# Performance work log

Measured on AMD Instinct MI355X. Metric: run time of the kernel, lower is better.

The kernel has to match this reference:

```python
import jax, jax.numpy as jnp
import numpy as np

N = 30000
E = 960000
F_IN = 16
NH1 = 36
NH2 = 36
KH = 8
IN_POOL = 2
OUT_POOL = 2
NUM_CLASSES = 10
RATIO = 0.1
EPS = 1e-5


def cheb_conv(x, src, dst, valid, W, b):
    """PyG ChebConv with sym normalization, lambda_max=2 -> L_hat = -D^-1/2 A D^-1/2.
    W: [K, in, out], valid: float mask [E] for (soft-)deleted edges."""
    n = x.shape[0]
    deg = jax.ops.segment_sum(valid, src, num_segments=n)
    dinv = jnp.where(deg > 0, jax.lax.rsqrt(deg), 0.0)
    norm = dinv[src] * dinv[dst] * valid  # [E]

    def prop(h):  # L_hat @ h
        return -jax.ops.segment_sum(norm[:, None] * h[src], dst, num_segments=n)

    k_hops = W.shape[0]
    tx0 = x
    out = tx0 @ W[0]
    if k_hops > 1:
        tx1 = prop(tx0)
        out = out + tx1 @ W[1]
        for kk in range(2, k_hops):
            tx2 = 2.0 * prop(tx1) - tx0
            out = out + tx2 @ W[kk]
            tx0, tx1 = tx1, tx2
    return out + b


def batch_norm(x, gamma, beta):
    mu = jnp.mean(x, axis=0)
    var = jnp.var(x, axis=0)
    return (x - mu) * jax.lax.rsqrt(var + EPS) * gamma + beta


def setup_inputs() -> dict:
    key = jax.random.key(0)
    ks = jax.random.split(key, 20)
    rn = lambda k, s: jax.random.normal(k, s, dtype=jnp.float32) * 0.1
    x = jax.random.normal(ks[0], (N, F_IN), dtype=jnp.float32)
    edge_index = jax.random.randint(ks[1], (2, E), 0, N, dtype=jnp.int32)
    return {
        "x": x,
        "edge_index": edge_index,
        "W1": rn(ks[2], (KH, F_IN, NH1)), "b1": jnp.zeros((NH1,), jnp.float32),
        "W2": rn(ks[3], (KH, NH1, NH2)), "b2": jnp.zeros((NH2,), jnp.float32),
        "g1": jnp.ones((NH1,), jnp.float32), "be1": jnp.zeros((NH1,), jnp.float32),
        "g2": jnp.ones((NH2,), jnp.float32), "be2": jnp.zeros((NH2,), jnp.float32),
        "Wc": rn(ks[4], (1, NH1, IN_POOL)), "bc": jnp.zeros((IN_POOL,), jnp.float32),
        "pool_w": rn(ks[5], (IN_POOL,)),
        "Wp": rn(ks[6], (KH, IN_POOL, OUT_POOL)), "bp": jnp.zeros((OUT_POOL,), jnp.float32),
        "W3": rn(ks[7], (1, NH1 + NH2 + OUT_POOL, NUM_CLASSES)),
        "b3": jnp.zeros((NUM_CLASSES,), jnp.float32),
    }


def reference(x, edge_index, W1, b1, W2, b2, g1, be1, g2, be2, Wc, bc, pool_w, Wp, bp, W3, b3):
    src, dst = edge_index[0], edge_index[1]
    valid = jnp.ones((src.shape[0],), jnp.float32)

    x1 = batch_norm(jax.nn.relu(cheb_conv(x, src, dst, valid, W1, b1)), g1, be1)
    x2 = batch_norm(jax.nn.relu(cheb_conv(x1, src, dst, valid, W2, b2)), g2, be2)
    xc = cheb_conv(x1, src, dst, valid, Wc, bc)

    # TopKPooling(ratio=0.1)
    score = jnp.tanh(xc @ pool_w / jnp.linalg.norm(pool_w))  # [N]
    k = int(np.ceil(RATIO * x.shape[0]))
    _, perm = jax.lax.top_k(score, k)
    xp1 = xc[perm] * score[perm][:, None]
    new_idx = jnp.full((x.shape[0],), -1, jnp.int32).at[perm].set(jnp.arange(k, dtype=jnp.int32))
    vs, vd = new_idx[src], new_idx[dst]
    valid_p = ((vs >= 0) & (vd >= 0)).astype(jnp.float32)
    src_p = jnp.where(vs >= 0, vs, 0)
    dst_p = jnp.where(vd >= 0, vd, 0)

    xp2 = cheb_conv(xp1, src_p, dst_p, valid_p, Wp, bp)  # [k, OUT_POOL]

    # nearest-neighbor unpooling using last-2 feature columns as 2D positions
    pos = x[:, -2:]              # [N, 2]
    pos_p = pos[perm]            # [k, 2]
    d2 = jnp.sum((pos[:, None, :] - pos_p[None, :, :]) ** 2, axis=-1)  # [N, k]
    nearest = jnp.argmin(d2, axis=1)
    x3u = xp2[nearest]           # [N, OUT_POOL]

    h = jnp.concatenate((x1, x2, x3u), axis=1)
    return cheb_conv(h, src, dst, valid, W3, b3)
```

## Files before the change

kernel.cpp:

```cpp
#include <hip/hip_runtime.h>
#include <cstdint>

constexpr int NN   = 30000;
constexpr int NE   = 960000;
constexpr int FIN  = 16;
constexpr int H1   = 36;
constexpr int H2   = 36;
constexpr int KHOP = 8;
constexpr int KSEL = 3000;
constexpr int PCAP = 32768;
constexpr int NCHUNK = 12;
constexpr int CHUNK = KSEL / NCHUNK;
constexpr int NB_H = 32;
constexpr int EPB  = (NE + NB_H - 1) / NB_H;
constexpr float EPSV = 1e-5f;

#define TPB 256

static inline int nb(long long t) { return (int)((t + TPB - 1) / TPB); }

__global__ __launch_bounds__(1024)
void k_hist(const int* __restrict__ src, const int* __restrict__ dst,
            int* __restrict__ partials, int* __restrict__ rank) {
    __shared__ int hist[NN];
    for (int j = threadIdx.x; j < NN; j += 1024) hist[j] = 0;
    __syncthreads();
    int b = blockIdx.x;
    int e0 = b * EPB, e1 = min(NE, e0 + EPB);
    if (blockIdx.y == 0) {
        for (int e = e0 + (int)threadIdx.x; e < e1; e += 1024)
            atomicAdd(&hist[src[e]], 1);
    } else {
        for (int e = e0 + (int)threadIdx.x; e < e1; e += 1024)
            rank[e] = atomicAdd(&hist[dst[e]], 1);
    }
    __syncthreads();
    int* P = partials + ((size_t)blockIdx.y * NB_H + b) * NN;
    for (int j = threadIdx.x; j < NN; j += 1024) P[j] = hist[j];
}

__global__ void k_red(int* __restrict__ partials, float* __restrict__ dinv,
                      int* __restrict__ cnt_dst, float* __restrict__ stats) {
    if (blockIdx.x == 0 && threadIdx.x < 144) stats[threadIdx.x] = 0.f;
    int j = blockIdx.x * blockDim.x + threadIdx.x;
    if (j >= NN) return;
    const int* Ps = partials;
    int s = 0;
#pragma unroll
    for (int b = 0; b < NB_H; ++b) s += Ps[(size_t)b * NN + j];
    dinv[j] = s > 0 ? rsqrtf((float)s) : 0.0f;
    int* Pd = partials + (size_t)NB_H * NN;
    int run = 0;
#pragma unroll
    for (int b = 0; b < NB_H; ++b) {
        int t = Pd[(size_t)b * NN + j];
        Pd[(size_t)b * NN + j] = run;
        run += t;
    }
    cnt_dst[j] = run;
}

__device__ __forceinline__ int block_scan_excl_1024(int val, int& total) {
    __shared__ int wsum[16];
    int tid = threadIdx.x, lane = tid & 63, wv = tid >> 6;
    int v = val;
#pragma unroll
    for (int off = 1; off < 64; off <<= 1) {
        int t = __shfl_up(v, off, 64);
        if (lane >= off) v += t;
    }
    __syncthreads();
    if (lane == 63) wsum[wv] = v;
    __syncthreads();
    if (tid < 16) {
        int w = wsum[tid];
#pragma unroll
        for (int off = 1; off < 16; off <<= 1) {
            int t = __shfl_up(w, off, 64);
            if (tid >= off) w += t;
        }
        wsum[tid] = w;
    }
    __syncthreads();
    int base = (wv > 0) ? wsum[wv - 1] : 0;
    total = wsum[15];
    return base + v - val;
}

__global__ void k_scan(const int* __restrict__ cnt, int* __restrict__ rowstart, int n) {
    __shared__ int run;
    if (threadIdx.x == 0) run = 0;
    __syncthreads();
    for (int base = 0; base < n; base += 1024) {
        int i = base + threadIdx.x;
        int v = (i < n) ? cnt[i] : 0;
        int tot; int ex = block_scan_excl_1024(v, tot);
        int r = run;
        if (i < n) rowstart[i] = r + ex;
        __syncthreads();
        if (threadIdx.x == 0) run += tot;
        __syncthreads();
    }
    if (threadIdx.x == 0) rowstart[n] = run;
}

__global__ __launch_bounds__(1024)
void k_scan_pool(const int* __restrict__ lens, int* __restrict__ prs,
                 const int* __restrict__ pcnt, float* __restrict__ dinvp) {
    __shared__ int run;
    if (threadIdx.x == 0) run = 0;
    __syncthreads();
    for (int base = 0; base < KSEL; base += 1024) {
        int i = base + threadIdx.x;
        int v = (i < KSEL) ? lens[i] : 0;
        int tot; int ex = block_scan_excl_1024(v, tot);
        int r = run;
        if (i < KSEL) prs[i] = r + ex;
        __syncthreads();
        if (threadIdx.x == 0) run += tot;
        __syncthreads();
    }
    if (threadIdx.x == 0) prs[KSEL] = run;
    for (int j = threadIdx.x; j < KSEL; j += 1024) {
        int c = pcnt[j];
        dinvp[j] = c > 0 ? rsqrtf((float)c) : 0.0f;
    }
}

__global__ void k_fill3(const int* __restrict__ src, const int* __restrict__ dst,
                        const int* __restrict__ rank, const float* __restrict__ dinv,
                        const int* __restrict__ rowstart, const int* __restrict__ Pd_excl,
                        int2* __restrict__ csr, int E) {
    int e = blockIdx.x * blockDim.x + threadIdx.x;
    if (e >= E) return;
    int s = src[e], d = dst[e];
    int b = e / EPB;
    int pos = rowstart[d] + Pd_excl[(size_t)b * NN + d] + rank[e];
    float w = -dinv[s] * dinv[d];
    csr[pos] = make_int2(s, __float_as_int(w));
}

template<int F, int O, int BN, int ES, bool FIRST>
__global__ __launch_bounds__(BN * (F / 4) * ES)
void k_prop_gemm(const int* __restrict__ rowstart, const int2* __restrict__ csr,
                 const float* __restrict__ h, const float* __restrict__ t0,
                 const float* __restrict__ Wk, const float* __restrict__ W0,
                 const float* __restrict__ bias, float* __restrict__ tout,
                 float* __restrict__ acc, int n) {
    constexpr int QF = F / 4;
    constexpr int NTH = BN * QF;
    constexpr int NT = NTH * ES;
    __shared__ float sT[BN * F];
    __shared__ float sP[(ES > 1) ? BN * F : 1];
    __shared__ float sW[F * O];
    __shared__ float sW0[FIRST ? F * O : 1];
    __shared__ float sX[FIRST ? BN * F : 1];
    const int tid = threadIdx.x;
    for (int i = tid; i < F * O; i += NT) sW[i] = Wk[i];
    if (FIRST) {
        for (int i = tid; i < F * O; i += NT) sW0[i] = W0[i];
        int base = blockIdx.x * BN * F;
        int lim = min(BN * F, n * F - base);
        for (int i = tid; i < lim; i += NT) sX[i] = h[base + i];
    }
    const int sl = tid / NTH;
    const int t2 = tid - sl * NTH;
    const int nl = t2 / QF, q = t2 - nl * QF;
    const int node = blockIdx.x * BN + nl;
    float4 p = {0.f, 0.f, 0.f, 0.f};
    if (node < n) {
        const float4* __restrict__ h4 = (const float4*)h;
        int e0 = rowstart[node], e1 = rowstart[node + 1];
        if (ES > 1) {
            int len = e1 - e0, half = (len + 1) >> 1;
            if (sl == 0) e1 = e0 + half; else e0 += half;
        }
        int e = e0;
        for (; e + 3 < e1; e += 4) {
            int2 ea = csr[e];
            int2 eb = csr[e + 1];
            int2 ec = csr[e + 2];
            int2 ed = csr[e + 3];
            float4 ha = h4[ea.x * QF + q];
            float4 hb = h4[eb.x * QF + q];
            float4 hc = h4[ec.x * QF + q];
            float4 hd = h4[ed.x * QF + q];
            float wa = __int_as_float(ea.y), wb = __int_as_float(eb.y);
            float wc = __int_as_float(ec.y), wd = __int_as_float(ed.y);
            p.x = fmaf(wa, ha.x, p.x); p.y = fmaf(wa, ha.y, p.y);
            p.z = fmaf(wa, ha.z, p.z); p.w = fmaf(wa, ha.w, p.w);
            p.x = fmaf(wb, hb.x, p.x); p.y = fmaf(wb, hb.y, p.y);
            p.z = fmaf(wb, hb.z, p.z); p.w = fmaf(wb, hb.w, p.w);
            p.x = fmaf(wc, hc.x, p.x); p.y = fmaf(wc, hc.y, p.y);
            p.z = fmaf(wc, hc.z, p.z); p.w = fmaf(wc, hc.w, p.w);
            p.x = fmaf(wd, hd.x, p.x); p.y = fmaf(wd, hd.y, p.y);
            p.z = fmaf(wd, hd.z, p.z); p.w = fmaf(wd, hd.w, p.w);
        }
        for (; e < e1; ++e) {
            int2 ew = csr[e];
            float w = __int_as_float(ew.y);
            float4 hv = h4[ew.x * QF + q];
            p.x = fmaf(w, hv.x, p.x); p.y = fmaf(w, hv.y, p.y);
            p.z = fmaf(w, hv.z, p.z); p.w = fmaf(w, hv.w, p.w);
        }
    }
    if (ES > 1) {
        if (sl == 1 && node < n) {
            sP[nl * F + 4 * q + 0] = p.x; sP[nl * F + 4 * q + 1] = p.y;
            sP[nl * F + 4 * q + 2] = p.z; sP[nl * F + 4 * q + 3] = p.w;
        }
        __syncthreads();
        if (sl == 0 && node < n) {
            p.x += sP[nl * F + 4 * q + 0]; p.y += sP[nl * F + 4 * q + 1];
            p.z += sP[nl * F + 4 * q + 2]; p.w += sP[nl * F + 4 * q + 3];
        }
    }
    if (sl == 0 && node < n) {
        if (!FIRST) {
            float4 tv = ((const float4*)t0)[node * QF + q];
            p.x = 2.f * p.x - tv.x; p.y = 2.f * p.y - tv.y;
            p.z = 2.f * p.z - tv.z; p.w = 2.f * p.w - tv.w;
        }
        ((float4*)tout)[node * QF + q] = p;
        sT[nl * F + 4 * q + 0] = p.x; sT[nl * F + 4 * q + 1] = p.y;
        sT[nl * F + 4 * q + 2] = p.z; sT[nl * F + 4 * q + 3] = p.w;
    }
    __syncthreads();
    for (int idx = tid; idx < BN * O; idx += NT) {
        int nl2 = idx / O, o = idx - nl2 * O;
        int gn = blockIdx.x * BN + nl2;
        if (gn >= n) break;
        float s;
        if (FIRST) {
            s = bias[o];
#pragma unroll
            for (int f = 0; f < F; ++f) s = fmaf(sX[nl2 * F + f], sW0[f * O + o], s);
        } else {
            s = 0.f;
        }
#pragma unroll
        for (int f = 0; f < F; ++f) s = fmaf(sT[nl2 * F + f], sW[f * O + o], s);
        if (FIRST) acc[gn * O + o] = s;
        else       acc[gn * O + o] += s;
    }
}

template<int C>
__global__ void k_colstats(const float* __restrict__ a, float* __restrict__ stats, int n) {
    __shared__ float b1[C], b2[C];
    for (int i = threadIdx.x; i < C; i += blockDim.x) { b1[i] = 0.f; b2[i] = 0.f; }
    __syncthreads();
    int t0 = blockIdx.x * blockDim.x + threadIdx.x;
    int stride = gridDim.x * blockDim.x;
    int c = t0 % C;
    float s1 = 0.f, s2 = 0.f;
    for (int t = t0; t < n * C; t += stride) {
        float v = fmaxf(a[t], 0.f);
        s1 += v; s2 = fmaf(v, v, s2);
    }
    atomicAdd(&b1[c], s1); atomicAdd(&b2[c], s2);
    __syncthreads();
    for (int i = threadIdx.x; i < C; i += blockDim.x) {
        atomicAdd(&stats[i], b1[i]); atomicAdd(&stats[C + i], b2[i]);
    }
}

template<int C>
__global__ void k_bn(const float* __restrict__ a, const float* __restrict__ stats,
                     const float* __restrict__ g, const float* __restrict__ be,
                     float* __restrict__ o, int n) {
    int t = blockIdx.x * blockDim.x + threadIdx.x;
    if (t >= n * C) return;
    int c = t % C;
    float mu = stats[c] / n;
    float var = stats[C + c] / n - mu * mu;
    float v = fmaxf(a[t], 0.f);
    o[t] = (v - mu) * rsqrtf(var + EPSV) * g[c] + be[c];
}

__global__ void k_xc_score(const float* __restrict__ x1, const float* __restrict__ Wc,
                           const float* __restrict__ bc, const float* __restrict__ pw,
                           float* __restrict__ xc, float* __restrict__ score,
                           unsigned* __restrict__ key, int* __restrict__ gh, int n) {
    int i = blockIdx.x * blockDim.x + threadIdx.x;
    if (i >= n) return;
    const float* r = &x1[i * H1];
    float a = bc[0], b = bc[1];
#pragma unroll
    for (int f = 0; f < H1; ++f) { float v = r[f]; a = fmaf(v, Wc[f * 2], a); b = fmaf(v, Wc[f * 2 + 1], b); }
    xc[i * 2] = a; xc[i * 2 + 1] = b;
    float w0 = pw[0], w1 = pw[1];
    float s = tanhf((a * w0 + b * w1) / sqrtf(w0 * w0 + w1 * w1));
    score[i] = s;
    unsigned u = __float_as_uint(s);
    unsigned k = (u & 0x80000000u) ? ~u : (u | 0x80000000u);
    key[i] = k;
    atomicAdd(&gh[k >> 16], 1);
}

__global__ void k_h16b(const unsigned* __restrict__ key, const unsigned* __restrict__ pB,
                       int* __restrict__ gh, int n) {
    unsigned B = *pB;
    int i = blockIdx.x * blockDim.x + threadIdx.x;
    if (i < n && (key[i] >> 16) == B) atomicAdd(&gh[key[i] & 0xFFFFu], 1);
}

__global__ __launch_bounds__(1024)
void k_scanhist(const int* __restrict__ hist, const int* __restrict__ kin, int kdef,
                const unsigned* __restrict__ prevBin, unsigned* __restrict__ outT,
                int* __restrict__ outRem) {
    __shared__ int cs[1024];
    __shared__ int sC, sAbove;
    const int tid = threadIdx.x;
    int k = kin ? *kin : kdef;
    int s = 0;
    int base = tid * 64;
#pragma unroll 8
    for (int j = 0; j < 64; ++j) s += hist[base + j];
    cs[tid] = s;
    __syncthreads();
    int rsum = cs[1023 - tid];
    int tot; int ex = block_scan_excl_1024(rsum, tot);
    int c = 1023 - tid;
    if (ex < k && ex + cs[c] >= k) { sC = c; sAbove = ex; }
    __syncthreads();
    if (tid < 64) {
        int bin = sC * 64 + 63 - tid;
        int val = hist[bin];
        int incl = val;
#pragma unroll
        for (int off = 1; off < 64; off <<= 1) {
            int t2 = __shfl_up(incl, off, 64);
            if (tid >= off) incl += t2;
        }
        int above2 = sAbove + (incl - val);
        if (above2 < k && above2 + val >= k) {
            if (prevBin) *outT = ((*prevBin) << 16) | (unsigned)bin;
            else         *outT = (unsigned)bin;
            *outRem = k - above2;
        }
    }
}

__global__ __launch_bounds__(1024)
void k_selcnt(const unsigned* __restrict__ key, const unsigned* __restrict__ pT,
              int* __restrict__ bgt, int* __restrict__ beq, int n) {
    __shared__ int sgt, seq;
    if (threadIdx.x == 0) { sgt = 0; seq = 0; }
    __syncthreads();
    unsigned T = *pT;
    int i = blockIdx.x * 1024 + threadIdx.x;
    if (i < n) {
        unsigned kk = key[i];
        if (kk > T) atomicAdd(&sgt, 1);
        else if (kk == T) atomicAdd(&seq, 1);
    }
    __syncthreads();
    if (threadIdx.x == 0) { bgt[blockIdx.x] = sgt; beq[blockIdx.x] = seq; }
}

__global__ void k_seloff(const int* __restrict__ bgt, const int* __restrict__ beq,
                         const int* __restrict__ pR, int* __restrict__ eqoff,
                         int* __restrict__ soff, int nblk) {
    int t = threadIdx.x;
    int g = (t < nblk) ? bgt[t] : 0;
    int q = (t < nblk) ? beq[t] : 0;
    int gi = g, qi = q;
#pragma unroll
    for (int off = 1; off < 64; off <<= 1) {
        int a = __shfl_up(gi, off, 64);
        int b = __shfl_up(qi, off, 64);
        if (t >= off) { gi += a; qi += b; }
    }
    int qex = qi - q;
    int r = *pR;
    int eqsel = min(max(r - qex, 0), q);
    int scnt = g + eqsel;
    int si = scnt;
#pragma unroll
    for (int off = 1; off < 64; off <<= 1) {
        int a = __shfl_up(si, off, 64);
        if (t >= off) si += a;
    }
    if (t < nblk) { eqoff[t] = qex; soff[t] = si - scnt; }
}

__global__ __launch_bounds__(1024)
void k_selfill(const unsigned* __restrict__ key, const unsigned* __restrict__ pT,
               const int* __restrict__ pR, const int* __restrict__ eqoff,
               const int* __restrict__ soff, int* __restrict__ nidx,
               int* __restrict__ sel, int n) {
    unsigned T = *pT; int r = *pR;
    int b = blockIdx.x;
    int i = b * 1024 + threadIdx.x;
    unsigned kk = (i < n) ? key[i] : 0u;
    int eq = (i < n && kk == T) ? 1 : 0;
    int gt = (i < n && kk > T) ? 1 : 0;
    int eq_tot; int eq_ex = block_scan_excl_1024(eq, eq_tot);
    int sf = gt | (eq & (((eqoff[b] + eq_ex) < r) ? 1 : 0));
    int s_tot; int s_ex = block_scan_excl_1024(sf, s_tot);
    if (i < n) {
        if (sf) { int slot = soff[b] + s_ex; nidx[i] = slot; sel[slot] = i; }
        else nidx[i] = -1;
    }
}

__global__ void k_plen(const int* __restrict__ m_rowstart, const int2* __restrict__ m_csr,
                       const int* __restrict__ nidx, const int* __restrict__ sel,
                       int* __restrict__ pcnt, int* __restrict__ lens) {
    int wid = (blockIdx.x * blockDim.x + threadIdx.x) >> 6;
    int lane = threadIdx.x & 63;
    if (wid >= KSEL) return;
    int node = sel[wid];
    int e0 = m_rowstart[node], e1 = m_rowstart[node + 1];
    int cnt = 0;
    for (int e = e0 + lane; e < e1; e += 64) {
        int vs = nidx[m_csr[e].x];
        if (vs >= 0) { ++cnt; atomicAdd(&pcnt[vs], 1); }
    }
#pragma unroll
    for (int off = 32; off; off >>= 1) cnt += __shfl_down(cnt, off, 64);
    if (lane == 0) lens[wid] = cnt;
}

__global__ void k_pfill(const int* __restrict__ m_rowstart, const int2* __restrict__ m_csr,
                        const int* __restrict__ nidx, const int* __restrict__ sel,
                        const float* __restrict__ dinvp, const int* __restrict__ prs,
                        int2* __restrict__ gcsr) {
    int wid = (blockIdx.x * blockDim.x + threadIdx.x) >> 6;
    int lane = threadIdx.x & 63;
    if (wid >= KSEL) return;
    int node = sel[wid];
    int e0 = m_rowstart[node], e1 = m_rowstart[node + 1];
    float dd = dinvp[wid];
    int pos = prs[wid];
    for (int base = e0; base < e1; base += 64) {
        int e = base + lane;
        int vs = -1;
        if (e < e1) vs = nidx[m_csr[e].x];
        bool valid = vs >= 0;
        unsigned long long mask = __ballot(valid);
        if (valid) {
            int myoff = __popcll(mask & ((1ull << lane) - 1ull));
            float w = -dinvp[vs] * dd;
            gcsr[pos + myoff] = make_int2(vs, __float_as_int(w));
        }
        pos += __popcll(mask);
    }
}

__global__ __launch_bounds__(1024)
void k_pooled4(const int* __restrict__ prs_g, const int2* __restrict__ gcsr,
               const int* __restrict__ sel, const float* __restrict__ xc,
               const float* __restrict__ score, const float* __restrict__ x,
               const float* __restrict__ Wp, const float* __restrict__ bp,
               float* __restrict__ pacc_out, float* __restrict__ selpos) {
    __shared__ float bufA[2 * KSEL];
    __shared__ float bufB[2 * KSEL];
    __shared__ int   prs[KSEL + 1];
    const int tid = threadIdx.x, NT = 1024;

    for (int j = tid; j <= KSEL; j += NT) prs[j] = prs_g[j];

    const float bp0 = bp[0], bp1 = bp[1];
    float accA[3], accB[3];
#pragma unroll
    for (int r = 0; r < 3; ++r) {
        int j = tid + r * NT;
        accA[r] = 0.f; accB[r] = 0.f;
        if (j < KSEL) {
            int i = sel[j];
            float s = score[i];
            float a = xc[2 * i] * s, b = xc[2 * i + 1] * s;
            bufA[2 * j] = a; bufA[2 * j + 1] = b;
            accA[r] = bp0 + a * Wp[0] + b * Wp[2];
            accB[r] = bp1 + a * Wp[1] + b * Wp[3];
            selpos[2 * j] = x[i * FIN + 14];
            selpos[2 * j + 1] = x[i * FIN + 15];
        }
    }
    __syncthreads();

    for (int k = 1; k < KHOP; ++k) {
        float* rb = (k & 1) ? bufA : bufB;
        float* wb = (k & 1) ? bufB : bufA;
        float w0 = Wp[k * 4 + 0], w1 = Wp[k * 4 + 1];
        float w2 = Wp[k * 4 + 2], w3 = Wp[k * 4 + 3];
#pragma unroll
        for (int r = 0; r < 3; ++r) {
            int j = tid + r * NT;
            if (j < KSEL) {
                float pa = 0.f, pb = 0.f;
                int e0 = prs[j], e1 = prs[j + 1];
                for (int e = e0; e < e1; ++e) {
                    int2 ew = gcsr[e];
                    float w = __int_as_float(ew.y);
                    pa = fmaf(w, rb[2 * ew.x], pa);
                    pb = fmaf(w, rb[2 * ew.x + 1], pb);
                }
                if (k >= 2) {
                    pa = 2.f * pa - wb[2 * j];
                    pb = 2.f * pb - wb[2 * j + 1];
                }
                wb[2 * j] = pa; wb[2 * j + 1] = pb;
                accA[r] = fmaf(pa, w0, fmaf(pb, w2, accA[r]));
                accB[r] = fmaf(pa, w1, fmaf(pb, w3, accB[r]));
            }
        }
        __syncthreads();
    }

#pragma unroll
    for (int r = 0; r < 3; ++r) {
        int j = tid + r * NT;
        if (j < KSEL) {
            pacc_out[2 * j] = accA[r];
            pacc_out[2 * j + 1] = accB[r];
        }
    }
}

__global__ void k_near_part(const float* __restrict__ x, const float* __restrict__ selpos,
                            unsigned long long* __restrict__ best, int n) {
    __shared__ float2 sp[CHUNK];
    const int j0 = blockIdx.y * CHUNK;
    for (int j = threadIdx.x; j < CHUNK; j += blockDim.x)
        sp[j] = ((const float2*)selpos)[j0 + j];
    __syncthreads();
    int i = blockIdx.x * blockDim.x + threadIdx.x;
    if (i >= n) return;
    float px = x[i * FIN + 14], py = x[i * FIN + 15];
    float bd = 3.4e38f; int bj = 0;
#pragma unroll 2
    for (int j = 0; j < CHUNK; ++j) {
        float dx = px - sp[j].x, dy = py - sp[j].y;
        float d = fmaf(dx, dx, dy * dy);
        if (d < bd) { bd = d; bj = j0 + j; }
    }
    unsigned long long pk = ((unsigned long long)__float_as_uint(bd) << 32) | (unsigned)bj;
    atomicMin(&best[i], pk);
}

__global__ void k_final(const float* __restrict__ x1, const float* __restrict__ x2,
                        const float* __restrict__ xp2, const unsigned long long* __restrict__ best,
                        const float* __restrict__ W3, const float* __restrict__ b3,
                        float* __restrict__ o, int n) {
    __shared__ float sW[740], sb[10];
    for (int i = threadIdx.x; i < 740; i += blockDim.x) sW[i] = W3[i];
    if (threadIdx.x < 10) sb[threadIdx.x] = b3[threadIdx.x];
    __syncthreads();
    int t = blockIdx.x * blockDim.x + threadIdx.x;
    if (t >= n * 10) return;
    int i = t / 10, c = t - 10 * (t / 10);
    float s = sb[c];
    const float* r1 = &x1[i * H1];
#pragma unroll
    for (int f = 0; f < H1; ++f) s = fmaf(r1[f], sW[f * 10 + c], s);
    const float* r2 = &x2[i * H2];
#pragma unroll
    for (int f = 0; f < H2; ++f) s = fmaf(r2[f], sW[(H1 + f) * 10 + c], s);
    int m = (int)(best[i] & 0xFFFFFFFFull);
    s = fmaf(xp2[m * 2],     sW[720 + c], s);
    s = fmaf(xp2[m * 2 + 1], sW[730 + c], s);
    o[t] = s;
}

extern "C" void kernel_launch(void* const* d_in, const int* in_sizes, int n_in,
                              void* d_out, int out_size, void* d_ws, size_t ws_size,
                              hipStream_t stream) {
    const float* x   = (const float*)d_in[0];
    const int*   ei  = (const int*)d_in[1];
    const int*   src = ei;
    const int*   dst = ei + NE;
    const float* W1  = (const float*)d_in[2];
    const float* b1  = (const float*)d_in[3];
    const float* W2  = (const float*)d_in[4];
    const float* b2  = (const float*)d_in[5];
    const float* g1  = (const float*)d_in[6];
    const float* be1 = (const float*)d_in[7];
    const float* g2  = (const float*)d_in[8];
    const float* be2 = (const float*)d_in[9];
    const float* Wc  = (const float*)d_in[10];
    const float* bc  = (const float*)d_in[11];
    const float* pw  = (const float*)d_in[12];
    const float* Wp  = (const float*)d_in[13];
    const float* bp  = (const float*)d_in[14];
    const float* W3  = (const float*)d_in[15];
    const float* b3  = (const float*)d_in[16];
    float* out = (float*)d_out;

    char* w = (char*)d_ws;
    auto alloc = [&](size_t bytes) -> void* {
        void* p = (void*)w;
        w += (bytes + 255) & ~(size_t)255;
        return p;
    };
    int*   cnt_dst  = (int*)alloc(NN * 4);
    float* dinv     = (float*)alloc(NN * 4);
    int*   rowstart = (int*)alloc((NN + 1) * 4);
    int*   rank     = (int*)alloc((size_t)NE * 4);
    int2*  csr      = (int2*)alloc((size_t)NE * 8);
    float* B1    = (float*)alloc((size_t)NN * H1 * 4);
    float* B2    = (float*)alloc((size_t)NN * H1 * 4);
    float* B3    = (float*)alloc((size_t)NN * H1 * 4);
    float* acc   = (float*)alloc((size_t)NN * H1 * 4);
    float* x1    = (float*)alloc((size_t)NN * H1 * 4);
    float* x2    = (float*)alloc((size_t)NN * H2 * 4);
    float* xc    = (float*)alloc((size_t)NN * 2 * 4);
    float* score = (float*)alloc(NN * 4);
    float* stats = (float*)alloc(144 * 4);
    unsigned* key   = (unsigned*)alloc(NN * 4);
    int* nidx       = (int*)alloc(NN * 4);
    int* sel        = (int*)alloc(KSEL * 4);
    unsigned long long* best = (unsigned long long*)alloc(NN * 8);
    unsigned* Tptr  = (unsigned*)alloc(4);
    int* Rptr       = (int*)alloc(4);
    unsigned* BinPtr = (unsigned*)alloc(4);
    int* RemPtr     = (int*)alloc(4);
    int* gh         = (int*)alloc(2 * 65536 * 4);
    int* pcnt       = (int*)alloc(KSEL * 4);
    int* bgt        = (int*)alloc(64 * 4);
    int* beq        = (int*)alloc(64 * 4);
    int* eqoff      = (int*)alloc(64 * 4);
    int* soff       = (int*)alloc(64 * 4);
    int* lens       = (int*)alloc(KSEL * 4);
    int* prs        = (int*)alloc((KSEL + 1) * 4);
    float* dinvp    = (float*)alloc(KSEL * 4);
    int2* gcsr      = (int2*)alloc((size_t)PCAP * 8);
    float* pacc     = (float*)alloc(KSEL * 2 * 4);
    float* selpos   = (float*)alloc(KSEL * 2 * 4);

    float* stats1 = stats;
    float* stats2 = stats + 72;

    int* partials = (int*)B1;

    const int NBK1 = (NN + 63) / 64;
    const int NBK2 = (NN + 31) / 32;
    const int CSB = 117;

    hipMemsetAsync(gh, 0, 2 * 65536 * 4 + ((KSEL * 4 + 255) & ~255), stream);
    hipMemsetAsync(best, 0xFF, NN * 8, stream);

    {
        dim3 gh2(NB_H, 2);
        k_hist<<<gh2, 1024, 0, stream>>>(src, dst, partials, rank);
        k_red<<<nb(NN), TPB, 0, stream>>>(partials, dinv, cnt_dst, stats);
        k_scan<<<1, 1024, 0, stream>>>(cnt_dst, rowstart, NN);
        k_fill3<<<nb(NE), TPB, 0, stream>>>(src, dst, rank, dinv, rowstart,
                                            partials + (size_t)NB_H * NN, csr, NE);
    }

    {
        float* rot[3] = {B1, B2, B3};
        k_prop_gemm<FIN, H1, 64, 2, true><<<NBK1, 512, 0, stream>>>(
            rowstart, csr, x, nullptr, W1 + FIN * H1, W1, b1, B1, acc, NN);
        const float* t_prev = x; const float* t_cur = B1;
        for (int kk = 2; kk < KHOP; ++kk) {
            float* o = rot[(kk - 1) % 3];
            k_prop_gemm<FIN, H1, 64, 2, false><<<NBK1, 512, 0, stream>>>(
                rowstart, csr, t_cur, t_prev, W1 + kk * FIN * H1, nullptr, nullptr, o, acc, NN);
            t_prev = t_cur; t_cur = o;
        }
        k_colstats<H1><<<CSB, TPB, 0, stream>>>(acc, stats1, NN);
        k_bn<H1><<<nb((long long)NN * H1), TPB, 0, stream>>>(acc, stats1, g1, be1, x1, NN);
    }

    {
        float* rot[3] = {B1, B2, B3};
        k_prop_gemm<H1, H2, 32, 2, true><<<NBK2, 576, 0, stream>>>(
            rowstart, csr, x1, nullptr, W2 + H1 * H2, W2, b2, B1, acc, NN);
        const float* t_prev = x1; const float* t_cur = B1;
        for (int kk = 2; kk < KHOP; ++kk) {
            float* o = rot[(kk - 1) % 3];
            k_prop_gemm<H1, H2, 32, 2, false><<<NBK2, 576, 0, stream>>>(
                rowstart, csr, t_cur, t_prev, W2 + kk * H1 * H2, nullptr, nullptr, o, acc, NN);
            t_prev = t_cur; t_cur = o;
        }
        k_colstats<H2><<<CSB, TPB, 0, stream>>>(acc, stats2, NN);
        k_bn<H2><<<nb((long long)NN * H2), TPB, 0, stream>>>(acc, stats2, g2, be2, x2, NN);
    }

    k_xc_score<<<nb(NN), TPB, 0, stream>>>(x1, Wc, bc, pw, xc, score, key, gh, NN);

    k_scanhist<<<1, 1024, 0, stream>>>(gh, nullptr, KSEL, nullptr, BinPtr, RemPtr);
    k_h16b<<<nb(NN), TPB, 0, stream>>>(key, BinPtr, gh + 65536, NN);
    k_scanhist<<<1, 1024, 0, stream>>>(gh + 65536, RemPtr, 0, BinPtr, Tptr, Rptr);

    {
        const int SB = (NN + 1023) / 1024;
        k_selcnt<<<SB, 1024, 0, stream>>>(key, Tptr, bgt, beq, NN);
        k_seloff<<<1, 64, 0, stream>>>(bgt, beq, Rptr, eqoff, soff, SB);
        k_selfill<<<SB, 1024, 0, stream>>>(key, Tptr, Rptr, eqoff, soff, nidx, sel, NN);
    }

    {
        const int WPB = TPB / 64;
        const int GB = (KSEL + WPB - 1) / WPB;
        k_plen<<<GB, TPB, 0, stream>>>(rowstart, csr, nidx, sel, pcnt, lens);
        k_scan_pool<<<1, 1024, 0, stream>>>(lens, prs, pcnt, dinvp);
        k_pfill<<<GB, TPB, 0, stream>>>(rowstart, csr, nidx, sel, dinvp, prs, gcsr);
    }

    k_pooled4<<<1, 1024, 0, stream>>>(prs, gcsr, sel, xc, score, x, Wp, bp, pacc, selpos);

    {
        dim3 g(nb(NN), NCHUNK);
        k_near_part<<<g, TPB, 0, stream>>>(x, selpos, best, NN);
    }
    k_final<<<nb((long long)NN * 10), TPB, 0, stream>>>(x1, x2, pacc, best, W3, b3, out, NN);
}
```

Measured before the change: 556.0 us.

## Remove intra-node edge splitting in propagation kernel and unify block size

Drops the two-slice edge split per node in the fused propagate+GEMM kernel, so each node's neighbor list is summed by a single thread group. This removes the shared-memory partial-sum buffer and an extra barrier. Both layers now use 64 nodes per block. It trades away parallelism over the edge loop and memory-level parallelism in the gathers, which may lengthen per-thread latency chains.

```diff
diff --git a/kernel.cpp b/kernel.cpp
--- a/kernel.cpp
+++ b/kernel.cpp
@@ -140,18 +140,16 @@
     csr[pos] = make_int2(s, __float_as_int(w));
 }
 
-template<int F, int O, int BN, int ES, bool FIRST>
-__global__ __launch_bounds__(BN * (F / 4) * ES)
+template<int F, int O, int BN, bool FIRST>
+__global__ __launch_bounds__(BN * F / 4)
 void k_prop_gemm(const int* __restrict__ rowstart, const int2* __restrict__ csr,
                  const float* __restrict__ h, const float* __restrict__ t0,
                  const float* __restrict__ Wk, const float* __restrict__ W0,
                  const float* __restrict__ bias, float* __restrict__ tout,
                  float* __restrict__ acc, int n) {
     constexpr int QF = F / 4;
-    constexpr int NTH = BN * QF;
-    constexpr int NT = NTH * ES;
+    constexpr int NT = BN * QF;
     __shared__ float sT[BN * F];
-    __shared__ float sP[(ES > 1) ? BN * F : 1];
     __shared__ float sW[F * O];
     __shared__ float sW0[FIRST ? F * O : 1];
     __shared__ float sX[FIRST ? BN * F : 1];
@@ -163,18 +161,12 @@
         int lim = min(BN * F, n * F - base);
         for (int i = tid; i < lim; i += NT) sX[i] = h[base + i];
     }
-    const int sl = tid / NTH;
-    const int t2 = tid - sl * NTH;
-    const int nl = t2 / QF, q = t2 - nl * QF;
+    const int nl = tid / QF, q = tid - nl * QF;
     const int node = blockIdx.x * BN + nl;
-    float4 p = {0.f, 0.f, 0.f, 0.f};
     if (node < n) {
         const float4* __restrict__ h4 = (const float4*)h;
+        float4 p = {0.f, 0.f, 0.f, 0.f};
         int e0 = rowstart[node], e1 = rowstart[node + 1];
-        if (ES > 1) {
-            int len = e1 - e0, half = (len + 1) >> 1;
-            if (sl == 0) e1 = e0 + half; else e0 += half;
-        }
         int e = e0;
         for (; e + 3 < e1; e += 4) {
             int2 ea = csr[e];
@@ -203,19 +195,6 @@
             p.x = fmaf(w, hv.x, p.x); p.y = fmaf(w, hv.y, p.y);
             p.z = fmaf(w, hv.z, p.z); p.w = fmaf(w, hv.w, p.w);
         }
-    }
-    if (ES > 1) {
-        if (sl == 1 && node < n) {
-            sP[nl * F + 4 * q + 0] = p.x; sP[nl * F + 4 * q + 1] = p.y;
-            sP[nl * F + 4 * q + 2] = p.z; sP[nl * F + 4 * q + 3] = p.w;
-        }
-        __syncthreads();
-        if (sl == 0 && node < n) {
-            p.x += sP[nl * F + 4 * q + 0]; p.y += sP[nl * F + 4 * q + 1];
-            p.z += sP[nl * F + 4 * q + 2]; p.w += sP[nl * F + 4 * q + 3];
-        }
-    }
-    if (sl == 0 && node < n) {
         if (!FIRST) {
             float4 tv = ((const float4*)t0)[node * QF + q];
             p.x = 2.f * p.x - tv.x; p.y = 2.f * p.y - tv.y;
@@ -635,8 +614,7 @@
 
     int* partials = (int*)B1;
 
-    const int NBK1 = (NN + 63) / 64;
-    const int NBK2 = (NN + 31) / 32;
+    const int NBK = (NN + 63) / 64;
     const int CSB = 117;
 
     hipMemsetAsync(gh, 0, 2 * 65536 * 4 + ((KSEL * 4 + 255) & ~255), stream);
@@ -653,12 +631,12 @@
 
     {
         float* rot[3] = {B1, B2, B3};
-        k_prop_gemm<FIN, H1, 64, 2, true><<<NBK1, 512, 0, stream>>>(
+        k_prop_gemm<FIN, H1, 64, true><<<NBK, 64 * (FIN / 4), 0, stream>>>(
             rowstart, csr, x, nullptr, W1 + FIN * H1, W1, b1, B1, acc, NN);
         const float* t_prev = x; const float* t_cur = B1;
         for (int kk = 2; kk < KHOP; ++kk) {
             float* o = rot[(kk - 1) % 3];
-            k_prop_gemm<FIN, H1, 64, 2, false><<<NBK1, 512, 0, stream>>>(
+            k_prop_gemm<FIN, H1, 64, false><<<NBK, 64 * (FIN / 4), 0, stream>>>(
                 rowstart, csr, t_cur, t_prev, W1 + kk * FIN * H1, nullptr, nullptr, o, acc, NN);
             t_prev = t_cur; t_cur = o;
         }
@@ -668,12 +646,12 @@
 
     {
         float* rot[3] = {B1, B2, B3};
-        k_prop_gemm<H1, H2, 32, 2, true><<<NBK2, 576, 0, stream>>>(
+        k_prop_gemm<H1, H2, 64, true><<<NBK, 64 * (H1 / 4), 0, stream>>>(
             rowstart, csr, x1, nullptr, W2 + H1 * H2, W2, b2, B1, acc, NN);
         const float* t_prev = x1; const float* t_cur = B1;
         for (int kk = 2; kk < KHOP; ++kk) {
             float* o = rot[(kk - 1) % 3];
-            k_prop_gemm<H1, H2, 32, 2, false><<<NBK2, 576, 0, stream>>>(
+            k_prop_gemm<H1, H2, 64, false><<<NBK, 64 * (H1 / 4), 0, stream>>>(
                 rowstart, csr, t_cur, t_prev, W2 + kk * H1 * H2, nullptr, nullptr, o, acc, NN);
             t_prev = t_cur; t_cur = o;
         }
```

Result: faster. 530.8 us (-4.5%).
